# Performance work log

Hardware: AMD Instinct MI355X
Metric: run time of the kernel (lower is better)

Reference implementation:

```python
import jax, jax.numpy as jnp
import numpy as np
from jax import lax

B, T, V, E, H, C, K = 256, 512, 50000, 128, 256, 128, 2


def setup_inputs() -> dict:
    key = jax.random.key(0)
    ks = jax.random.split(key, 16)
    s = lambda *sh: 1.0 / np.sqrt(sh[0])
    return {
        "input_current": jax.random.randint(ks[0], (B, T), 0, V, dtype=jnp.int32),
        "input_left": jax.random.randint(ks[1], (B, T), 0, V, dtype=jnp.int32),
        "input_right": jax.random.randint(ks[2], (B, T), 0, V, dtype=jnp.int32),
        "emb": jax.random.normal(ks[3], (V, E), jnp.float32) * 0.05,
        "Wf": jax.random.normal(ks[4], (E, H), jnp.float32) * s(E),
        "Uf": jax.random.normal(ks[5], (H, H), jnp.float32) * s(H),
        "bf": jnp.zeros((H,), jnp.float32),
        "Wb": jax.random.normal(ks[6], (E, H), jnp.float32) * s(E),
        "Ub": jax.random.normal(ks[7], (H, H), jnp.float32) * s(H),
        "bb": jnp.zeros((H,), jnp.float32),
        "Wc": jax.random.normal(ks[8], (2 * H + E, C), jnp.float32) * s(2 * H + E),
        "bc": jnp.zeros((C,), jnp.float32),
        "Wd": jax.random.normal(ks[9], (C, K), jnp.float32) * s(C),
        "bd": jnp.zeros((K,), jnp.float32),
    }


def _simple_rnn(x, W, U, b):
    # x: [B,T,E] -> outputs [B,T,H]; h_t = tanh(x_t W + b + h_{t-1} U)
    xw = jnp.einsum("bte,eh->bth", x, W) + b  # precompute input projection
    h0 = jnp.zeros((x.shape[0], U.shape[0]), x.dtype)

    def step(h, xw_t):
        h = jnp.tanh(xw_t + h @ U)
        return h, h

    _, hs = lax.scan(step, h0, jnp.swapaxes(xw, 0, 1))  # scan over time
    return jnp.swapaxes(hs, 0, 1)


def reference(input_current, input_left, input_right, emb, Wf, Uf, bf, Wb, Ub, bb, Wc, bc, Wd, bd):
    e_cur = emb[input_current]  # [B,T,E]
    e_left = emb[input_left]
    e_right = emb[input_right]
    x_left = _simple_rnn(e_left, Wf, Uf, bf)  # [B,T,H]
    # go_backwards RNN: process reversed sequence, then model reverses back
    x_right = _simple_rnn(e_right[:, ::-1], Wb, Ub, bb)[:, ::-1]  # [B,T,H]
    x = jnp.concatenate([x_left, e_cur, x_right], axis=2)  # [B,T,2H+E]
    x = jnp.tanh(jnp.einsum("btd,dc->btc", x, Wc) + bc)  # Conv1D k=1 + tanh
    x = jnp.max(x, axis=1)  # GlobalMaxPooling1D
    return jax.nn.sigmoid(x @ Wd + bd)  # [B,K]
```

## Files before the change

kernel.cpp:

```cpp
#include <hip/hip_runtime.h>
#include <hip/hip_bf16.h>


#define B_ 256
#define T_ 512
#define E_ 128
#define H_ 256
#define C_ 128

typedef __attribute__((ext_vector_type(8))) short short8;
typedef __attribute__((ext_vector_type(4))) float float4v;
typedef __attribute__((ext_vector_type(2))) unsigned int uint2v;

__device__ inline unsigned short f2bf(float f) {
  unsigned u = __float_as_uint(f);
  u += 0x7fffu + ((u >> 16) & 1u);
  return (unsigned short)(u >> 16);
}
__device__ inline unsigned pkbf(float a, float b) {
  __hip_bfloat162 h2 = __float22bfloat162_rn(float2{a, b});
  union { __hip_bfloat162 h; unsigned u; } cv;
  cv.h = h2;
  return cv.u;
}
__device__ inline float lo16f(unsigned u) { return __uint_as_float(u << 16); }
__device__ inline float hi16f(unsigned u) { return __uint_as_float(u & 0xffff0000u); }
__device__ inline float fast_tanh(float x) {
  float e = __expf(2.f * x);
  float r = __builtin_amdgcn_rcpf(e + 1.f);
  return __builtin_fmaf(-2.f, r, 1.f);
}
__device__ inline unsigned enc_f(float f) {
  unsigned u = __float_as_uint(f);
  return (u & 0x80000000u) ? ~u : (u | 0x80000000u);
}
__device__ inline float dec_f(unsigned key) {
  unsigned bits = (key & 0x80000000u) ? (key ^ 0x80000000u) : ~key;
  return __uint_as_float(bits);
}
__device__ inline void sync_lds() {
  asm volatile("s_waitcnt lgkmcnt(0)\n\ts_barrier" ::: "memory");
}

__device__ inline void st_agent(unsigned short* p, uint2v v) {
  union { uint2v v2; unsigned long long u; } cv;
  cv.v2 = v;
  __hip_atomic_store(reinterpret_cast<unsigned long long*>(p), cv.u,
                     __ATOMIC_RELAXED, __HIP_MEMORY_SCOPE_AGENT);
}

__device__ inline void wait_flag_ge(const int* f, int v) {
  if (__hip_atomic_load(f, __ATOMIC_RELAXED, __HIP_MEMORY_SCOPE_AGENT) < v) {
    while (__hip_atomic_load(f, __ATOMIC_RELAXED, __HIP_MEMORY_SCOPE_AGENT) <
           v)
      __builtin_amdgcn_s_sleep(8);
  }
  (void)__hip_atomic_load(f, __ATOMIC_ACQUIRE, __HIP_MEMORY_SCOPE_AGENT);
}

__global__ __launch_bounds__(256) void prep_kernel(
    const float* __restrict__ Wf, const float* __restrict__ Wb,
    const float* __restrict__ Wc, const float* __restrict__ Uf,
    const float* __restrict__ Ub,
    unsigned short* __restrict__ WfT, unsigned short* __restrict__ WbT,
    unsigned short* __restrict__ WcT, unsigned short* __restrict__ UfT,
    unsigned short* __restrict__ UbT, unsigned int* __restrict__ pooled,
    int* __restrict__ flags) {
  int gid = blockIdx.x * 256 + threadIdx.x;
  int stride = gridDim.x * 256;
  for (int i = gid; i < 128 * 256; i += stride) {
    int k = i >> 8, n = i & 255;
    WfT[n * 128 + k] = f2bf(Wf[i]);
    WbT[n * 128 + k] = f2bf(Wb[i]);
  }
  for (int i = gid; i < 640 * 128; i += stride) {
    int k = i >> 7, n = i & 127;
    WcT[n * 640 + k] = f2bf(Wc[i]);
  }
  for (int i = gid; i < 256 * 256; i += stride) {
    int k = i >> 8, n = i & 255;
    UfT[n * 256 + k] = f2bf(Uf[i]);
    UbT[n * 256 + k] = f2bf(Ub[i]);
  }
  for (int i = gid; i < B_ * C_; i += stride) pooled[i] = 0u;
  for (int i = gid; i < 1024; i += stride) flags[i] = 0;
}

__global__ __launch_bounds__(512, 1) void fused_kernel(
    const int* __restrict__ idxL, const int* __restrict__ idxR,
    const int* __restrict__ idxC, const float* __restrict__ emb,
    const unsigned short* __restrict__ WfT,
    const unsigned short* __restrict__ WbT,
    const float* __restrict__ bfv, const float* __restrict__ bbv,
    const unsigned short* __restrict__ UfT,
    const unsigned short* __restrict__ UbT,
    const unsigned short* __restrict__ WcT, const float* __restrict__ bc,
    unsigned short* x, unsigned int* __restrict__ pooled,
    int* __restrict__ flags) {
  const int blk = blockIdx.x;
  const int tid = threadIdx.x;
  const int lane = tid & 63, q = lane >> 4, l15 = lane & 15;

  __shared__ __attribute__((aligned(16))) unsigned short hbuf[2][16][280];

  if (blk < 32) {
    const int dir = blk & 1;
    const int btile = blk >> 1;
    const int b0 = btile * 16;
    const unsigned short* __restrict__ UT = dir ? UbT : UfT;
    const int xoff = dir ? 384 : 0;
    const int tstep = dir ? -1 : 1;
    const int t0 = dir ? (T_ - 1) : 0;
    const ptrdiff_t dstep = (ptrdiff_t)tstep * 640;
    const int wv = tid >> 6;
    int* fl = flags + (dir * 16 + btile) * 32;

    unsigned short* hb0 = &hbuf[0][0][0];
    unsigned short* hb1 = &hbuf[1][0][0];
    for (int i = tid; i < 16 * 280; i += 512) hb0[i] = 0;

    short8 ufr[2][8];
#pragma unroll
    for (int mt = 0; mt < 2; ++mt)
#pragma unroll
      for (int kt = 0; kt < 8; ++kt)
        ufr[mt][kt] = *(const short8*)(UT + (32 * wv + 16 * mt + l15) * H_ +
                                       kt * 32 + q * 8);

    int lastc = dir ? 31 : 0;
    wait_flag_ge(fl + lastc, 1);

    unsigned short* ptrS[2];
    const unsigned short* ptrL[2];
    uint2v curA[2], curB[2], infA[2], infB[2];
#pragma unroll
    for (int mt = 0; mt < 2; ++mt) {
      unsigned short* base =
          x + (size_t)(b0 + 2 * wv + mt) * T_ * 640 + xoff + lane * 4;
      unsigned short* bt = base + (ptrdiff_t)t0 * 640;
      curA[mt] = *(const uint2v*)(bt);
      curB[mt] = *(const uint2v*)(bt + dstep);
      infA[mt] = *(const uint2v*)(bt + 2 * dstep);
      infB[mt] = *(const uint2v*)(bt + 3 * dstep);
      ptrS[mt] = bt;
      ptrL[mt] = bt + 4 * dstep;
    }

    const unsigned lrd = l15 * 280;
    const unsigned lwr = l15 * 280 + 32 * wv;

    __syncthreads();

#pragma unroll 1
    for (int p = 0; p < 256; ++p) {
      int c = dir ? ((506 - 2 * p) >> 4) : ((2 * p + 5) >> 4);
      c = c < 0 ? 0 : (c > 31 ? 31 : c);
      if (c != lastc) {
        wait_flag_ge(fl + c, 1);
        lastc = c;
      }
      uint2v ldA[2], ldB[2];
      if (p < 254) {
#pragma unroll
        for (int mt = 0; mt < 2; ++mt) {
          ldA[mt] = *(const uint2v*)(ptrL[mt]);
          ldB[mt] = *(const uint2v*)(ptrL[mt] + dstep);
        }
      } else {
#pragma unroll
        for (int mt = 0; mt < 2; ++mt) {
          ldA[mt] = infA[mt];
          ldB[mt] = infB[mt];
        }
      }
#pragma unroll
      for (int mt = 0; mt < 2; ++mt) ptrL[mt] += 2 * dstep;

      {
        short8 afr[8];
#pragma unroll
        for (int kt = 0; kt < 8; ++kt)
          afr[kt] = *(const short8*)(hb0 + lrd + kt * 32 + q * 8);
        float4v acc[2];
#pragma unroll
        for (int mt = 0; mt < 2; ++mt)
          acc[mt] = (float4v){lo16f(curA[mt].x), hi16f(curA[mt].x),
                              lo16f(curA[mt].y), hi16f(curA[mt].y)};
#pragma unroll
        for (int kt = 0; kt < 8; ++kt)
#pragma unroll
          for (int mt = 0; mt < 2; ++mt)
            acc[mt] = __builtin_amdgcn_mfma_f32_16x16x32_bf16(
                ufr[mt][kt], afr[kt], acc[mt], 0, 0, 0);
#pragma unroll
        for (int mt = 0; mt < 2; ++mt) {
          uint2v hv = {pkbf(fast_tanh(acc[mt][0]), fast_tanh(acc[mt][1])),
                       pkbf(fast_tanh(acc[mt][2]), fast_tanh(acc[mt][3]))};
          *(uint2v*)(hb1 + lwr + 16 * mt + 4 * q) = hv;
          st_agent(ptrS[mt], hv);
        }
      }
      sync_lds();

      {
        short8 afr[8];
#pragma unroll
        for (int kt = 0; kt < 8; ++kt)
          afr[kt] = *(const short8*)(hb1 + lrd + kt * 32 + q * 8);
        float4v acc[2];
#pragma unroll
        for (int mt = 0; mt < 2; ++mt)
          acc[mt] = (float4v){lo16f(curB[mt].x), hi16f(curB[mt].x),
                              lo16f(curB[mt].y), hi16f(curB[mt].y)};
#pragma unroll
        for (int kt = 0; kt < 8; ++kt)
#pragma unroll
          for (int mt = 0; mt < 2; ++mt)
            acc[mt] = __builtin_amdgcn_mfma_f32_16x16x32_bf16(
                ufr[mt][kt], afr[kt], acc[mt], 0, 0, 0);
#pragma unroll
        for (int mt = 0; mt < 2; ++mt) {
          uint2v hv = {pkbf(fast_tanh(acc[mt][0]), fast_tanh(acc[mt][1])),
                       pkbf(fast_tanh(acc[mt][2]), fast_tanh(acc[mt][3]))};
          *(uint2v*)(hb0 + lwr + 16 * mt + 4 * q) = hv;
          st_agent(ptrS[mt] + dstep, hv);
        }
      }
#pragma unroll
      for (int mt = 0; mt < 2; ++mt) {
        ptrS[mt] += 2 * dstep;
        curA[mt] = infA[mt];
        curB[mt] = infB[mt];
        infA[mt] = ldA[mt];
        infB[mt] = ldB[mt];
      }
      if (((p + 1) & 7) == 0) {
        asm volatile("s_waitcnt vmcnt(0) lgkmcnt(0)\n\ts_barrier" ::: "memory");
        if (tid == 0) {
          const int cdone = dir ? (32 - ((p + 1) >> 3)) : (((p + 1) >> 3) - 1);
          __hip_atomic_store(fl + cdone, 2, __ATOMIC_RELAXED,
                             __HIP_MEMORY_SCOPE_AGENT);
        }
      } else {
        sync_lds();
      }
    }
    return;
  }

  if (blk < 1056) {
    const int b2 = blk - 32;
    const int z = b2 >> 5, r = b2 & 31;
    const int btile = r & 15, dirg = r >> 4;
    const int chunk = dirg ? (31 - z) : z;
    const int w8 = tid >> 6;
    const int g = w8 >> 2, wv = w8 & 3;
    const int t0 = chunk * 16 + g * 8;
    const int b0 = btile * 16;
    const int* __restrict__ idx = dirg ? idxR : idxL;
    const unsigned short* __restrict__ WT = dirg ? WbT : WfT;
    const float* __restrict__ bias = dirg ? bbv : bfv;

    short8 wfr[4][4];
#pragma unroll
    for (int mt = 0; mt < 4; ++mt)
#pragma unroll
      for (int kt = 0; kt < 4; ++kt)
        wfr[mt][kt] = *(const short8*)(WT + (64 * wv + 16 * mt + l15) * 128 +
                                       kt * 32 + q * 8);
    float4v bv[4];
#pragma unroll
    for (int mt = 0; mt < 4; ++mt)
      bv[mt] = *(const float4v*)(bias + 64 * wv + 16 * mt + 4 * q);

    int er[8];
#pragma unroll
    for (int j = 0; j < 8; ++j) er[j] = idx[(b0 + l15) * T_ + t0 + j];

    float4v g0[8];
#pragma unroll
    for (int kt = 0; kt < 4; ++kt) {
      const float* p8 = emb + (size_t)er[0] * E_ + kt * 32 + q * 8;
      g0[2 * kt] = *(const float4v*)p8;
      g0[2 * kt + 1] = *(const float4v*)(p8 + 4);
    }

#pragma unroll 1
    for (int j = 0; j < 8; ++j) {
      float4v gn[8];
      if (j < 7) {
#pragma unroll
        for (int kt = 0; kt < 4; ++kt) {
          const float* p8 = emb + (size_t)er[j + 1] * E_ + kt * 32 + q * 8;
          gn[2 * kt] = *(const float4v*)p8;
          gn[2 * kt + 1] = *(const float4v*)(p8 + 4);
        }
      }
      short8 efr[4];
#pragma unroll
      for (int kt = 0; kt < 4; ++kt) {
        union { unsigned u[4]; short8 s; } cv;
        cv.u[0] = pkbf(g0[2 * kt][0], g0[2 * kt][1]);
        cv.u[1] = pkbf(g0[2 * kt][2], g0[2 * kt][3]);
        cv.u[2] = pkbf(g0[2 * kt + 1][0], g0[2 * kt + 1][1]);
        cv.u[3] = pkbf(g0[2 * kt + 1][2], g0[2 * kt + 1][3]);
        efr[kt] = cv.s;
      }
      float4v acc[4];
#pragma unroll
      for (int mt = 0; mt < 4; ++mt) acc[mt] = (float4v){0.f, 0.f, 0.f, 0.f};
#pragma unroll
      for (int kt = 0; kt < 4; ++kt)
#pragma unroll
        for (int mt = 0; mt < 4; ++mt)
          acc[mt] = __builtin_amdgcn_mfma_f32_16x16x32_bf16(
              wfr[mt][kt], efr[kt], acc[mt], 0, 0, 0);
      const int t = t0 + j;
#pragma unroll
      for (int mt = 0; mt < 4; ++mt) {
        float4v v = acc[mt] + bv[mt];
        uint2v pk = {pkbf(v[0], v[1]), pkbf(v[2], v[3])};
        st_agent(x + ((size_t)(b0 + 4 * wv + mt) * T_ + t) * 640 +
                     dirg * 384 + lane * 4,
                 pk);
      }
      if (j < 7) {
#pragma unroll
        for (int kk = 0; kk < 8; ++kk) g0[kk] = gn[kk];
      }
    }
    __syncthreads();
    if (tid == 0) {
      __hip_atomic_store(flags + (dirg * 16 + btile) * 32 + chunk, 1,
                         __ATOMIC_RELAXED, __HIP_MEMORY_SCOPE_AGENT);
    }
    return;
  }

  {
    extern __shared__ unsigned short dtile[];
    const int b2 = blk - 1056;
    const int btile = b2 & 15, g = b2 >> 4;
    const int b0 = btile * 16;
    const int w = tid >> 6;

    short8 wfr[20];
#pragma unroll
    for (int kt = 0; kt < 20; ++kt)
      wfr[kt] =
          *(const short8*)(WcT + (size_t)(16 * w + l15) * 640 + kt * 32 + q * 8);
    float4v bv = *(const float4v*)(bc + 16 * w + 4 * q);

    float4v mx = (float4v){-1e30f, -1e30f, -1e30f, -1e30f};

    const int* flF = flags + btile * 32;
    const int* flB = flags + (16 + btile) * 32;

    const int srow = tid >> 4;
    const int tt0 = srow >> 4, row0 = srow & 15;
    const int ssub = tid & 15;
    const int f0 = 16 * (row0 & 7) + 8 * (row0 >> 3);

#pragma unroll 1
    for (int s = 0; s < 4; ++s) {
      const int rk = g + 8 * s;
      const int c = (rk & 1) ? (16 + (rk >> 1)) : (15 - (rk >> 1));
      wait_flag_ge(flF + c, 2);
      wait_flag_ge(flB + c, 2);
      const int t0c = c * 16;

      auto stage = [&](int jp, int buf) {
        const int t = t0c + 2 * jp + tt0;
        const unsigned short* src = x + ((size_t)(b0 + row0) * T_ + t) * 640;
        unsigned short* dst =
            dtile + (size_t)((buf * 2 + tt0) * 16 + row0) * 648;
        *(short8*)(dst + ssub * 8) = *(const short8*)(src + ssub * 8);
        *(short8*)(dst + 128 + ssub * 8) = *(const short8*)(src + 128 + ssub * 8);
        *(short8*)(dst + 384 + ssub * 8) = *(const short8*)(src + 384 + ssub * 8);
        *(short8*)(dst + 512 + ssub * 8) = *(const short8*)(src + 512 + ssub * 8);
        const int er = idxC[(b0 + ssub) * T_ + t];
        const float* ep = emb + (size_t)er * E_ + f0;
        float4v e0 = *(const float4v*)ep;
        float4v e1 = *(const float4v*)(ep + 4);
        *(uint2v*)(dst + 256 + 4 * ssub) =
            (uint2v){pkbf(e0[0], e0[1]), pkbf(e0[2], e0[3])};
        *(uint2v*)(dst + 320 + 4 * ssub) =
            (uint2v){pkbf(e1[0], e1[1]), pkbf(e1[2], e1[3])};
      };

      stage(0, 0);
      __syncthreads();
#pragma unroll 1
      for (int jp = 0; jp < 8; ++jp) {
        const int buf = jp & 1;
        if (jp < 7) stage(jp + 1, buf ^ 1);
        float4v acc0 = (float4v){0.f, 0.f, 0.f, 0.f};
        float4v acc1 = acc0;
#pragma unroll
        for (int kt = 0; kt < 20; ++kt) {
          int rrow, so1, so2;
          if (kt < 8) {
            rrow = 2 * kt + (q >> 1);
            so1 = 128 * (q & 1) + 4 * l15;
            so2 = so1 + 64;
          } else if (kt < 12) {
            rrow = 2 * (kt - 8) + (q >> 1) + 8 * (q & 1);
            so1 = 256 + 4 * l15;
            so2 = 320 + 4 * l15;
          } else {
            rrow = 2 * (kt - 12) + (q >> 1);
            so1 = 384 + 128 * (q & 1) + 4 * l15;
            so2 = so1 + 64;
          }
          const unsigned short* r0p =
              dtile + (size_t)((buf * 2) * 16 + rrow) * 648;
          const unsigned short* r1p = r0p + 16 * 648;
          uint2v a1 = *(const uint2v*)(r0p + so1);
          uint2v a2 = *(const uint2v*)(r0p + so2);
          uint2v b1 = *(const uint2v*)(r1p + so1);
          uint2v b2 = *(const uint2v*)(r1p + so2);
          union { unsigned u[4]; short8 s8; } cva, cvb;
          cva.u[0] = a1.x; cva.u[1] = a1.y; cva.u[2] = a2.x; cva.u[3] = a2.y;
          cvb.u[0] = b1.x; cvb.u[1] = b1.y; cvb.u[2] = b2.x; cvb.u[3] = b2.y;
          acc0 = __builtin_amdgcn_mfma_f32_16x16x32_bf16(wfr[kt], cva.s8,
                                                         acc0, 0, 0, 0);
          acc1 = __builtin_amdgcn_mfma_f32_16x16x32_bf16(wfr[kt], cvb.s8,
                                                         acc1, 0, 0, 0);
        }
#pragma unroll
        for (int i = 0; i < 4; ++i)
          mx[i] = fmaxf(fmaxf(mx[i], acc0[i]), acc1[i]);
        __syncthreads();
      }
    }
#pragma unroll
    for (int i = 0; i < 4; ++i)
      atomicMax(pooled + (b0 + l15) * C_ + 16 * w + 4 * q + i,
                enc_f(fast_tanh(mx[i] + bv[i])));
  }
}

__global__ __launch_bounds__(256) void dense_kernel(
    const unsigned int* __restrict__ pooled, const float* __restrict__ Wd,
    const float* __restrict__ bd, float* __restrict__ out) {
  int b = threadIdx.x;
  float s0 = bd[0], s1 = bd[1];
#pragma unroll 4
  for (int c = 0; c < C_; ++c) {
    float f = dec_f(pooled[b * C_ + c]);
    s0 += f * Wd[c * 2 + 0];
    s1 += f * Wd[c * 2 + 1];
  }
  out[b * 2 + 0] = 1.f / (1.f + __expf(-s0));
  out[b * 2 + 1] = 1.f / (1.f + __expf(-s1));
}

extern "C" void kernel_launch(void* const* d_in, const int* in_sizes, int n_in,
                              void* d_out, int out_size, void* d_ws, size_t ws_size,
                              hipStream_t stream) {
  const int* idxC = (const int*)d_in[0];
  const int* idxL = (const int*)d_in[1];
  const int* idxR = (const int*)d_in[2];
  const float* emb = (const float*)d_in[3];
  const float* Wf = (const float*)d_in[4];
  const float* Uf = (const float*)d_in[5];
  const float* bf_ = (const float*)d_in[6];
  const float* Wb = (const float*)d_in[7];
  const float* Ub = (const float*)d_in[8];
  const float* bb_ = (const float*)d_in[9];
  const float* Wc = (const float*)d_in[10];
  const float* bc = (const float*)d_in[11];
  const float* Wd = (const float*)d_in[12];
  const float* bd = (const float*)d_in[13];

  char* ws = (char*)d_ws;
  unsigned short* x = (unsigned short*)ws;
  unsigned int* pooled = (unsigned int*)(ws + 167772160);
  unsigned short* WfT = (unsigned short*)(ws + 167903232);
  unsigned short* WbT = WfT + 256 * 128;
  unsigned short* WcT = WbT + 256 * 128;
  unsigned short* UfT = WcT + 128 * 640;
  unsigned short* UbT = UfT + 256 * 256;
  int* flags = (int*)(ws + 168460288);

  prep_kernel<<<64, 256, 0, stream>>>(Wf, Wb, Wc, Uf, Ub, WfT, WbT, WcT, UfT,
                                      UbT, pooled, flags);
  fused_kernel<<<1184, 512, 120 * 1024, stream>>>(idxL, idxR, idxC, emb, WfT,
                                                  WbT, bf_, bb_, UfT, UbT, WcT,
                                                  bc, x, pooled, flags);
  dense_kernel<<<1, 256, 0, stream>>>(pooled, Wd, bd, (float*)d_out);
}
```

Baseline: 556.3 us.

## Split recurrent MFMA chains, prefetch flags, defer chunk-done signalling, coalesce prep writes

```diff
diff --git a/kernel.cpp b/kernel.cpp
--- a/kernel.cpp
+++ b/kernel.cpp
@@ -68,19 +68,19 @@
     int* __restrict__ flags) {
   int gid = blockIdx.x * 256 + threadIdx.x;
   int stride = gridDim.x * 256;
-  for (int i = gid; i < 128 * 256; i += stride) {
-    int k = i >> 8, n = i & 255;
-    WfT[n * 128 + k] = f2bf(Wf[i]);
-    WbT[n * 128 + k] = f2bf(Wb[i]);
-  }
-  for (int i = gid; i < 640 * 128; i += stride) {
-    int k = i >> 7, n = i & 127;
-    WcT[n * 640 + k] = f2bf(Wc[i]);
+  for (int i = gid; i < 256 * 128; i += stride) {
+    int n = i >> 7, k = i & 127;
+    WfT[i] = f2bf(Wf[k * 256 + n]);
+    WbT[i] = f2bf(Wb[k * 256 + n]);
+  }
+  for (int i = gid; i < 128 * 640; i += stride) {
+    int n = i / 640, k = i - n * 640;
+    WcT[i] = f2bf(Wc[k * 128 + n]);
   }
   for (int i = gid; i < 256 * 256; i += stride) {
-    int k = i >> 8, n = i & 255;
-    UfT[n * 256 + k] = f2bf(Uf[i]);
-    UbT[n * 256 + k] = f2bf(Ub[i]);
+    int n = i >> 8, k = i & 255;
+    UfT[i] = f2bf(Uf[k * 256 + n]);
+    UbT[i] = f2bf(Ub[k * 256 + n]);
   }
   for (int i = gid; i < B_ * C_; i += stride) pooled[i] = 0u;
   for (int i = gid; i < 1024; i += stride) flags[i] = 0;
@@ -129,6 +129,9 @@
 
     int lastc = dir ? 31 : 0;
     wait_flag_ge(fl + lastc, 1);
+    int fpre = __hip_atomic_load(fl + (dir ? 30 : 1), __ATOMIC_ACQUIRE,
+                                 __HIP_MEMORY_SCOPE_AGENT);
+    int pending = -1;
 
     unsigned short* ptrS[2];
     const unsigned short* ptrL[2];
@@ -156,8 +159,13 @@
       int c = dir ? ((506 - 2 * p) >> 4) : ((2 * p + 5) >> 4);
       c = c < 0 ? 0 : (c > 31 ? 31 : c);
       if (c != lastc) {
-        wait_flag_ge(fl + c, 1);
+        if (fpre < 1) wait_flag_ge(fl + c, 1);
         lastc = c;
+        const int nc = c + (dir ? -1 : 1);
+        fpre = (nc >= 0 && nc < 32)
+                   ? __hip_atomic_load(fl + nc, __ATOMIC_ACQUIRE,
+                                       __HIP_MEMORY_SCOPE_AGENT)
+                   : 1;
       }
       uint2v ldA[2], ldB[2];
       if (p < 254) {
@@ -181,21 +189,27 @@
 #pragma unroll
         for (int kt = 0; kt < 8; ++kt)
           afr[kt] = *(const short8*)(hb0 + lrd + kt * 32 + q * 8);
-        float4v acc[2];
-#pragma unroll
-        for (int mt = 0; mt < 2; ++mt)
-          acc[mt] = (float4v){lo16f(curA[mt].x), hi16f(curA[mt].x),
-                              lo16f(curA[mt].y), hi16f(curA[mt].y)};
-#pragma unroll
-        for (int kt = 0; kt < 8; ++kt)
-#pragma unroll
-          for (int mt = 0; mt < 2; ++mt)
-            acc[mt] = __builtin_amdgcn_mfma_f32_16x16x32_bf16(
-                ufr[mt][kt], afr[kt], acc[mt], 0, 0, 0);
+        float4v accA[2], accB[2];
 #pragma unroll
         for (int mt = 0; mt < 2; ++mt) {
-          uint2v hv = {pkbf(fast_tanh(acc[mt][0]), fast_tanh(acc[mt][1])),
-                       pkbf(fast_tanh(acc[mt][2]), fast_tanh(acc[mt][3]))};
+          accA[mt] = (float4v){lo16f(curA[mt].x), hi16f(curA[mt].x),
+                               lo16f(curA[mt].y), hi16f(curA[mt].y)};
+          accB[mt] = (float4v){0.f, 0.f, 0.f, 0.f};
+        }
+#pragma unroll
+        for (int kt = 0; kt < 4; ++kt)
+#pragma unroll
+          for (int mt = 0; mt < 2; ++mt) {
+            accA[mt] = __builtin_amdgcn_mfma_f32_16x16x32_bf16(
+                ufr[mt][kt], afr[kt], accA[mt], 0, 0, 0);
+            accB[mt] = __builtin_amdgcn_mfma_f32_16x16x32_bf16(
+                ufr[mt][kt + 4], afr[kt + 4], accB[mt], 0, 0, 0);
+          }
+#pragma unroll
+        for (int mt = 0; mt < 2; ++mt) {
+          float4v s = accA[mt] + accB[mt];
+          uint2v hv = {pkbf(fast_tanh(s[0]), fast_tanh(s[1])),
+                       pkbf(fast_tanh(s[2]), fast_tanh(s[3]))};
           *(uint2v*)(hb1 + lwr + 16 * mt + 4 * q) = hv;
           st_agent(ptrS[mt], hv);
         }
@@ -207,21 +221,27 @@
 #pragma unroll
         for (int kt = 0; kt < 8; ++kt)
           afr[kt] = *(const short8*)(hb1 + lrd + kt * 32 + q * 8);
-        float4v acc[2];
-#pragma unroll
-        for (int mt = 0; mt < 2; ++mt)
-          acc[mt] = (float4v){lo16f(curB[mt].x), hi16f(curB[mt].x),
-                              lo16f(curB[mt].y), hi16f(curB[mt].y)};
-#pragma unroll
-        for (int kt = 0; kt < 8; ++kt)
-#pragma unroll
-          for (int mt = 0; mt < 2; ++mt)
-            acc[mt] = __builtin_amdgcn_mfma_f32_16x16x32_bf16(
-                ufr[mt][kt], afr[kt], acc[mt], 0, 0, 0);
+        float4v accA[2], accB[2];
 #pragma unroll
         for (int mt = 0; mt < 2; ++mt) {
-          uint2v hv = {pkbf(fast_tanh(acc[mt][0]), fast_tanh(acc[mt][1])),
-                       pkbf(fast_tanh(acc[mt][2]), fast_tanh(acc[mt][3]))};
+          accA[mt] = (float4v){lo16f(curB[mt].x), hi16f(curB[mt].x),
+                               lo16f(curB[mt].y), hi16f(curB[mt].y)};
+          accB[mt] = (float4v){0.f, 0.f, 0.f, 0.f};
+        }
+#pragma unroll
+        for (int kt = 0; kt < 4; ++kt)
+#pragma unroll
+          for (int mt = 0; mt < 2; ++mt) {
+            accA[mt] = __builtin_amdgcn_mfma_f32_16x16x32_bf16(
+                ufr[mt][kt], afr[kt], accA[mt], 0, 0, 0);
+            accB[mt] = __builtin_amdgcn_mfma_f32_16x16x32_bf16(
+                ufr[mt][kt + 4], afr[kt + 4], accB[mt], 0, 0, 0);
+          }
+#pragma unroll
+        for (int mt = 0; mt < 2; ++mt) {
+          float4v s = accA[mt] + accB[mt];
+          uint2v hv = {pkbf(fast_tanh(s[0]), fast_tanh(s[1])),
+                       pkbf(fast_tanh(s[2]), fast_tanh(s[3]))};
           *(uint2v*)(hb0 + lwr + 16 * mt + 4 * q) = hv;
           st_agent(ptrS[mt] + dstep, hv);
         }
@@ -235,16 +255,21 @@
         infB[mt] = ldB[mt];
       }
       if (((p + 1) & 7) == 0) {
-        asm volatile("s_waitcnt vmcnt(0) lgkmcnt(0)\n\ts_barrier" ::: "memory");
-        if (tid == 0) {
-          const int cdone = dir ? (32 - ((p + 1) >> 3)) : (((p + 1) >> 3) - 1);
-          __hip_atomic_store(fl + cdone, 2, __ATOMIC_RELAXED,
+        asm volatile("s_waitcnt vmcnt(16) lgkmcnt(0)\n\ts_barrier" :::
+                         "memory");
+        if (tid == 0 && pending >= 0)
+          __hip_atomic_store(fl + pending, 2, __ATOMIC_RELAXED,
                              __HIP_MEMORY_SCOPE_AGENT);
-        }
+        pending = dir ? (32 - ((p + 1) >> 3)) : (((p + 1) >> 3) - 1);
       } else {
         sync_lds();
       }
     }
+    asm volatile("s_waitcnt vmcnt(0)" ::: "memory");
+    __syncthreads();
+    if (tid == 0)
+      __hip_atomic_store(fl + pending, 2, __ATOMIC_RELAXED,
+                         __HIP_MEMORY_SCOPE_AGENT);
     return;
   }
 
@@ -440,10 +465,10 @@
   }
 }
 
-__global__ __launch_bounds__(256) void dense_kernel(
+__global__ __launch_bounds__(64) void dense_kernel(
     const unsigned int* __restrict__ pooled, const float* __restrict__ Wd,
     const float* __restrict__ bd, float* __restrict__ out) {
-  int b = threadIdx.x;
+  int b = blockIdx.x * 64 + threadIdx.x;
   float s0 = bd[0], s1 = bd[1];
 #pragma unroll 4
   for (int c = 0; c < C_; ++c) {
@@ -488,5 +513,5 @@
   fused_kernel<<<1184, 512, 120 * 1024, stream>>>(idxL, idxR, idxC, emb, WfT,
                                                   WbT, bf_, bb_, UfT, UbT, WcT,
                                                   bc, x, pooled, flags);
-  dense_kernel<<<1, 256, 0, stream>>>(pooled, Wd, bd, (float*)d_out);
-}
+  dense_kernel<<<4, 64, 0, stream>>>(pooled, Wd, bd, (float*)d_out);
+}
```

Result: no change. 546.3 us (-1.8%).
